# Kernel tuning notes

Hardware: AMD Instinct MI355X
Metric: run time of the kernel (lower is better)

The kernel has to match this reference:

```python
import jax, jax.numpy as jnp
import numpy as np

TEMPERATURE = 0.07
N_CLASSES = 100


def setup_inputs() -> dict:
    key = jax.random.key(0)
    k1, k2 = jax.random.split(key)
    N, D = 8192, 128
    emb = jax.random.normal(k1, (N, D), dtype=jnp.float32)
    # unit-normalize so exp(sim / temperature) stays finite in fp32
    emb = emb / jnp.linalg.norm(emb, axis=1, keepdims=True)
    labels = jax.random.randint(k2, (N,), 0, N_CLASSES, dtype=jnp.int64)
    return {"embeddings": emb, "labels": labels}


def reference(embeddings, labels):
    N = embeddings.shape[0]
    dt = embeddings.dtype
    # [N, N] similarity
    sim = jnp.matmul(embeddings, embeddings.T) / TEMPERATURE
    off_diag = 1.0 - jnp.eye(N, dtype=dt)
    pos_mask = (labels[:, None] == labels[None, :]).astype(dt) * off_diag
    exp_sim = jnp.exp(sim) * off_diag  # diagonal zeroed
    positive_sum = jnp.sum(exp_sim * pos_mask, axis=1)
    total_sum = jnp.sum(exp_sim, axis=1)
    loss = -jnp.log(positive_sum / (total_sum + 1e-8) + 1e-8)
    valid = pos_mask.sum(axis=1) > 0
    cnt = jnp.sum(valid.astype(dt))
    mean_loss = jnp.where(
        cnt > 0,
        jnp.sum(jnp.where(valid, loss, jnp.zeros_like(loss))) / jnp.maximum(cnt, 1.0),
        jnp.asarray(0.0, dtype=dt),
    )
    return mean_loss
```

## Files before the change

### kernel.cpp

```cpp
#include <hip/hip_runtime.h>

#define N 8192
#define D 128
#define SCALE_A 20.6098592f
#define NP 64
#define NBLK (NP * (NP + 1) / 2)

using short8  = __attribute__((ext_vector_type(8))) short;
using float4v = __attribute__((ext_vector_type(4))) float;

#if __has_builtin(__builtin_amdgcn_exp2f)
#define EXP2(x) __builtin_amdgcn_exp2f(x)
#else
#define EXP2(x) __expf((x) * 0.69314718f)
#endif

static __device__ inline unsigned int f2bf(float f) {
    union { float f; unsigned int u; } x;
    x.f = f;
    unsigned int u = x.u;
    return (u + 0x7FFFu + ((u >> 16) & 1u)) >> 16;
}

__global__ __launch_bounds__(256) void cl_prep(
    const float* __restrict__ emb, unsigned short* __restrict__ bfB,
    unsigned short* __restrict__ bfA, float* __restrict__ tot,
    int* __restrict__ ticket)
{
    const int t = blockIdx.x * 256 + threadIdx.x;
    const float* p = emb + (size_t)t * 16;
    uint4 ob[2], oa[2];
    #pragma unroll
    for (int h = 0; h < 2; ++h) {
        float4v f0 = *(const float4v*)(p + h * 8);
        float4v f1 = *(const float4v*)(p + h * 8 + 4);
        ob[h].x = f2bf(f0[0]) | (f2bf(f0[1]) << 16);
        ob[h].y = f2bf(f0[2]) | (f2bf(f0[3]) << 16);
        ob[h].z = f2bf(f1[0]) | (f2bf(f1[1]) << 16);
        ob[h].w = f2bf(f1[2]) | (f2bf(f1[3]) << 16);
        oa[h].x = f2bf(f0[0] * SCALE_A) | (f2bf(f0[1] * SCALE_A) << 16);
        oa[h].y = f2bf(f0[2] * SCALE_A) | (f2bf(f0[3] * SCALE_A) << 16);
        oa[h].z = f2bf(f1[0] * SCALE_A) | (f2bf(f1[1] * SCALE_A) << 16);
        oa[h].w = f2bf(f1[2] * SCALE_A) | (f2bf(f1[3] * SCALE_A) << 16);
    }
    ((uint4*)bfB)[t * 2]     = ob[0];
    ((uint4*)bfB)[t * 2 + 1] = ob[1];
    ((uint4*)bfA)[t * 2]     = oa[0];
    ((uint4*)bfA)[t * 2 + 1] = oa[1];
    if (t < 2 * N) tot[t] = 0.f;
    if (t == 0) *ticket = 0;
}

__global__ __launch_bounds__(512, 4) void cl_main(
    const unsigned short* __restrict__ bfA, const unsigned short* __restrict__ bfB,
    const int* __restrict__ labels,
    float* __restrict__ tot, float* __restrict__ pos,
    int* __restrict__ ticket, float* __restrict__ out)
{
    __shared__ uint4 ldsB[128 * 16];
    __shared__ float sred[2][8];
    __shared__ int   s_ticket;

    const int tid  = threadIdx.x;
    const int lane = tid & 63;
    const int wave = tid >> 6;
    const int q    = lane >> 4;
    const int c    = lane & 15;

    const int k = blockIdx.x;
    int bi = (int)((129.0f - sqrtf(16641.0f - 8.0f * (float)k)) * 0.5f);
    while (bi * (129 - bi) / 2 > k) --bi;
    while ((bi + 1) * (128 - bi) / 2 <= k) ++bi;
    const int bj = bi + (k - bi * (129 - bi) / 2);
    const int R0 = bi * 128, C0 = bj * 128;
    const bool diagblk = (bi == bj);

    const uint4* src = (const uint4*)bfB + (size_t)C0 * 16;
    #pragma unroll
    for (int i = 0; i < 4; ++i) {
        const int g     = tid + i * 512;
        const int row   = g >> 4;
        const int chunk = g & 15;
        __builtin_amdgcn_global_load_lds(
            (const __attribute__((address_space(1))) void*)(src + row * 16 + (chunk ^ (row & 15))),
            (__attribute__((address_space(3))) void*)(&ldsB[g]),
            16, 0, 0);
    }

    short8 afrag[4];
    int rowlab[4], collab[8];
    {
        const int arow = R0 + wave * 16 + c;
        #pragma unroll
        for (int ks = 0; ks < 4; ++ks)
            afrag[ks] = *(const short8*)(bfA + (size_t)arow * D + ks * 32 + q * 8);
        #pragma unroll
        for (int reg = 0; reg < 4; ++reg)
            rowlab[reg] = labels[R0 + wave * 16 + q * 4 + reg];
        #pragma unroll
        for (int tc = 0; tc < 8; ++tc)
            collab[tc] = labels[C0 + tc * 16 + c];
    }

    asm volatile("s_waitcnt vmcnt(0)" ::: "memory");
    __builtin_amdgcn_s_barrier();
    __builtin_amdgcn_sched_barrier(0);

    float4v acc[8];
    #pragma unroll
    for (int tc = 0; tc < 8; ++tc) {
        float4v z = {0.f, 0.f, 0.f, 0.f};
        acc[tc] = z;
    }
    const short8* ldsS = (const short8*)ldsB;
    #pragma unroll
    for (int ks = 0; ks < 4; ++ks) {
        const short8* pk = ldsS + c * 16 + ((ks * 4 + q) ^ c);
        #pragma unroll
        for (int tc = 0; tc < 8; ++tc) {
            if (diagblk && tc < wave) continue;
            short8 b = pk[tc * 256];
            acc[tc] = __builtin_amdgcn_mfma_f32_16x16x32_bf16(
                afrag[ks], b, acc[tc], 0, 0, 0);
        }
    }

    float tot_a[4] = {0.f, 0.f, 0.f, 0.f};
    float pos_a[4] = {0.f, 0.f, 0.f, 0.f};
    float ctot[8]  = {0.f, 0.f, 0.f, 0.f, 0.f, 0.f, 0.f, 0.f};
    float cpos[8]  = {0.f, 0.f, 0.f, 0.f, 0.f, 0.f, 0.f, 0.f};
    #pragma unroll
    for (int tc = 0; tc < 8; ++tc) {
        if (diagblk && tc < wave) continue;
        const int lc = collab[tc];
        if (diagblk && tc == wave) {
            #pragma unroll
            for (int reg = 0; reg < 4; ++reg) {
                float v = EXP2(acc[tc][reg]);
                if ((q * 4 + reg) >= c) v = 0.f;
                tot_a[reg] += v;  ctot[tc] += v;
                if (rowlab[reg] == lc) { pos_a[reg] += v; cpos[tc] += v; }
            }
        } else {
            #pragma unroll
            for (int reg = 0; reg < 4; ++reg) {
                float v = EXP2(acc[tc][reg]);
                tot_a[reg] += v;  ctot[tc] += v;
                if (rowlab[reg] == lc) { pos_a[reg] += v; cpos[tc] += v; }
            }
        }
    }

    #pragma unroll
    for (int reg = 0; reg < 4; ++reg) {
        float t = tot_a[reg];
        float p = pos_a[reg];
        #pragma unroll
        for (int m = 1; m < 16; m <<= 1) {
            t += __shfl_xor(t, m, 64);
            p += __shfl_xor(p, m, 64);
        }
        if (c == 0) {
            const int r = R0 + wave * 16 + q * 4 + reg;
            atomicAdd(&tot[r], t);
            atomicAdd(&pos[r], p);
        }
    }

    #pragma unroll
    for (int tc = 0; tc < 8; ++tc) {
        if (diagblk && tc < wave) continue;
        float t = ctot[tc], p = cpos[tc];
        t += __shfl_xor(t, 16, 64);  t += __shfl_xor(t, 32, 64);
        p += __shfl_xor(p, 16, 64);  p += __shfl_xor(p, 32, 64);
        if (q == 0) {
            const int cc = C0 + tc * 16 + c;
            atomicAdd(&tot[cc], t);
            atomicAdd(&pos[cc], p);
        }
    }

    asm volatile("s_waitcnt vmcnt(0)" ::: "memory");
    __syncthreads();
    if (tid == 0)
        s_ticket = __hip_atomic_fetch_add(ticket, 1, __ATOMIC_RELAXED,
                                          __HIP_MEMORY_SCOPE_AGENT);
    __syncthreads();
    if (s_ticket != NBLK - 1) return;

    float lsum = 0.f, lcnt = 0.f;
    #pragma unroll 4
    for (int i = tid; i < N; i += 512) {
        const float t = __hip_atomic_load(&tot[i], __ATOMIC_RELAXED,
                                          __HIP_MEMORY_SCOPE_AGENT);
        const float p = __hip_atomic_load(&pos[i], __ATOMIC_RELAXED,
                                          __HIP_MEMORY_SCOPE_AGENT);
        const float loss = -__logf(p / (t + 1e-8f) + 1e-8f);
        if (p > 0.f) { lsum += loss; lcnt += 1.f; }
    }
    #pragma unroll
    for (int m = 1; m < 64; m <<= 1) {
        lsum += __shfl_xor(lsum, m, 64);
        lcnt += __shfl_xor(lcnt, m, 64);
    }
    if (lane == 0) { sred[0][wave] = lsum; sred[1][wave] = lcnt; }
    __syncthreads();
    if (tid == 0) {
        float s = 0.f, n = 0.f;
        #pragma unroll
        for (int w = 0; w < 8; ++w) { s += sred[0][w]; n += sred[1][w]; }
        out[0] = (n > 0.f) ? s / fmaxf(n, 1.f) : 0.f;
    }
}

extern "C" void kernel_launch(void* const* d_in, const int* in_sizes, int n_in,
                              void* d_out, int out_size, void* d_ws, size_t ws_size,
                              hipStream_t stream) {
    const float* emb  = (const float*)d_in[0];
    const int* labels = (const int*)d_in[1];
    unsigned short* bfB = (unsigned short*)d_ws;
    unsigned short* bfA = bfB + (size_t)N * D;
    float* tot    = (float*)(bfA + (size_t)N * D);
    float* pos    = tot + N;
    int*   ticket = (int*)(pos + N);

    cl_prep<<<256, 256, 0, stream>>>(emb, bfB, bfA, tot, ticket);
    cl_main<<<NBLK, 512, 0, stream>>>(bfA, bfB, labels, tot, pos,
                                      ticket, (float*)d_out);
}
```

Measured before the change: 114.2 us.

## Make blocks persistent over row strips, reusing A fragments across column tiles

Replaces the 2080 independent upper-triangular tile blocks with 512 blocks. Each block owns one 128-row strip and walks 4–5 column tiles chosen by cyclic offset (a circulant symmetric covering), keeping the A fragments in registers and accumulating row sums across tiles. Row-sum atomics and A loads drop several-fold, and per-block launch and tile-index overhead goes away. In exchange, each block runs a serial loop where the next B tile is loaded only after the current tile is finished, with no double buffering, so load latency is exposed on every iteration. The cid==0 blocks for i<32 take one extra tile, which makes the work uneven across blocks.

```diff
diff --git a/kernel.cpp b/kernel.cpp
--- a/kernel.cpp
+++ b/kernel.cpp
@@ -4,7 +4,8 @@
 #define D 128
 #define SCALE_A 20.6098592f
 #define NP 64
-#define NBLK (NP * (NP + 1) / 2)
+#define NBLK 512
+#define NBLK_PREP 256
 
 using short8  = __attribute__((ext_vector_type(8))) short;
 using float4v = __attribute__((ext_vector_type(4))) float;
@@ -67,87 +68,138 @@
     const int q    = lane >> 4;
     const int c    = lane & 15;
 
-    const int k = blockIdx.x;
-    int bi = (int)((129.0f - sqrtf(16641.0f - 8.0f * (float)k)) * 0.5f);
-    while (bi * (129 - bi) / 2 > k) --bi;
-    while ((bi + 1) * (128 - bi) / 2 <= k) ++bi;
-    const int bj = bi + (k - bi * (129 - bi) / 2);
-    const int R0 = bi * 128, C0 = bj * 128;
-    const bool diagblk = (bi == bj);
-
-    const uint4* src = (const uint4*)bfB + (size_t)C0 * 16;
-    #pragma unroll
-    for (int i = 0; i < 4; ++i) {
-        const int g     = tid + i * 512;
-        const int row   = g >> 4;
-        const int chunk = g & 15;
-        __builtin_amdgcn_global_load_lds(
-            (const __attribute__((address_space(1))) void*)(src + row * 16 + (chunk ^ (row & 15))),
-            (__attribute__((address_space(3))) void*)(&ldsB[g]),
-            16, 0, 0);
+    const int i   = blockIdx.x >> 3;
+    const int cid = blockIdx.x & 7;
+    const int nit = (cid == 0 && i < 32) ? 5 : 4;
+    const int R0r = i * 128;
+    const uint4* bfB4 = (const uint4*)bfB;
+
+    int m0 = cid * 4;
+    {
+        const uint4* src = bfB4 + (size_t)(((i + m0) & 63) * 128) * 16;
+        #pragma unroll
+        for (int s = 0; s < 4; ++s) {
+            const int g     = tid + s * 512;
+            const int row   = g >> 4;
+            const int chunk = g & 15;
+            __builtin_amdgcn_global_load_lds(
+                (const __attribute__((address_space(1))) void*)(src + row * 16 + (chunk ^ (row & 15))),
+                (__attribute__((address_space(3))) void*)(&ldsB[g]),
+                16, 0, 0);
+        }
     }
 
     short8 afrag[4];
-    int rowlab[4], collab[8];
+    int rowlab[4];
     {
-        const int arow = R0 + wave * 16 + c;
+        const int arow = R0r + wave * 16 + c;
         #pragma unroll
         for (int ks = 0; ks < 4; ++ks)
             afrag[ks] = *(const short8*)(bfA + (size_t)arow * D + ks * 32 + q * 8);
         #pragma unroll
         for (int reg = 0; reg < 4; ++reg)
-            rowlab[reg] = labels[R0 + wave * 16 + q * 4 + reg];
-        #pragma unroll
-        for (int tc = 0; tc < 8; ++tc)
-            collab[tc] = labels[C0 + tc * 16 + c];
-    }
-
-    asm volatile("s_waitcnt vmcnt(0)" ::: "memory");
+            rowlab[reg] = labels[R0r + wave * 16 + q * 4 + reg];
+    }
+    int collab[8];
+    #pragma unroll
+    for (int tc = 0; tc < 8; ++tc)
+        collab[tc] = labels[((i + m0) & 63) * 128 + tc * 16 + c];
+
+    asm volatile("s_waitcnt vmcnt(0) lgkmcnt(0)" ::: "memory");
     __builtin_amdgcn_s_barrier();
     __builtin_amdgcn_sched_barrier(0);
 
-    float4v acc[8];
-    #pragma unroll
-    for (int tc = 0; tc < 8; ++tc) {
-        float4v z = {0.f, 0.f, 0.f, 0.f};
-        acc[tc] = z;
-    }
-    const short8* ldsS = (const short8*)ldsB;
-    #pragma unroll
-    for (int ks = 0; ks < 4; ++ks) {
-        const short8* pk = ldsS + c * 16 + ((ks * 4 + q) ^ c);
-        #pragma unroll
-        for (int tc = 0; tc < 8; ++tc) {
-            if (diagblk && tc < wave) continue;
-            short8 b = pk[tc * 256];
-            acc[tc] = __builtin_amdgcn_mfma_f32_16x16x32_bf16(
-                afrag[ks], b, acc[tc], 0, 0, 0);
-        }
-    }
-
     float tot_a[4] = {0.f, 0.f, 0.f, 0.f};
     float pos_a[4] = {0.f, 0.f, 0.f, 0.f};
-    float ctot[8]  = {0.f, 0.f, 0.f, 0.f, 0.f, 0.f, 0.f, 0.f};
-    float cpos[8]  = {0.f, 0.f, 0.f, 0.f, 0.f, 0.f, 0.f, 0.f};
-    #pragma unroll
-    for (int tc = 0; tc < 8; ++tc) {
-        if (diagblk && tc < wave) continue;
-        const int lc = collab[tc];
-        if (diagblk && tc == wave) {
+
+    #pragma unroll 1
+    for (int it = 0; it < nit; ++it) {
+        const int m    = (cid == 0) ? ((it == 4) ? 32 : it) : (cid * 4 + it);
+        const int j    = (i + m) & 63;
+        const int C0   = j * 128;
+        const bool diag = (m == 0);
+
+        float4v acc[8];
+        #pragma unroll
+        for (int tc = 0; tc < 8; ++tc) {
+            float4v z = {0.f, 0.f, 0.f, 0.f};
+            acc[tc] = z;
+        }
+        const short8* ldsS = (const short8*)ldsB;
+        #pragma unroll
+        for (int ks = 0; ks < 4; ++ks) {
+            const short8* pk = ldsS + c * 16 + ((ks * 4 + q) ^ c);
             #pragma unroll
-            for (int reg = 0; reg < 4; ++reg) {
-                float v = EXP2(acc[tc][reg]);
-                if ((q * 4 + reg) >= c) v = 0.f;
-                tot_a[reg] += v;  ctot[tc] += v;
-                if (rowlab[reg] == lc) { pos_a[reg] += v; cpos[tc] += v; }
-            }
-        } else {
+            for (int tc = 0; tc < 8; ++tc) {
+                if (diag && tc < wave) continue;
+                short8 b = pk[tc * 256];
+                acc[tc] = __builtin_amdgcn_mfma_f32_16x16x32_bf16(
+                    afrag[ks], b, acc[tc], 0, 0, 0);
+            }
+        }
+
+        float ctot[8] = {0,0,0,0,0,0,0,0};
+        float cpos[8] = {0,0,0,0,0,0,0,0};
+        #pragma unroll
+        for (int tc = 0; tc < 8; ++tc) {
+            if (diag && tc < wave) continue;
+            const int lc = collab[tc];
+            if (diag && tc == wave) {
+                #pragma unroll
+                for (int reg = 0; reg < 4; ++reg) {
+                    float v = EXP2(acc[tc][reg]);
+                    if ((q * 4 + reg) >= c) v = 0.f;
+                    tot_a[reg] += v;  ctot[tc] += v;
+                    if (rowlab[reg] == lc) { pos_a[reg] += v; cpos[tc] += v; }
+                }
+            } else {
+                #pragma unroll
+                for (int reg = 0; reg < 4; ++reg) {
+                    float v = EXP2(acc[tc][reg]);
+                    tot_a[reg] += v;  ctot[tc] += v;
+                    if (rowlab[reg] == lc) { pos_a[reg] += v; cpos[tc] += v; }
+                }
+            }
+        }
+
+        #pragma unroll
+        for (int tc = 0; tc < 8; ++tc) {
+            if (diag && tc < wave) continue;
+            float t = ctot[tc], p = cpos[tc];
+            t += __shfl_xor(t, 16, 64);  t += __shfl_xor(t, 32, 64);
+            p += __shfl_xor(p, 16, 64);  p += __shfl_xor(p, 32, 64);
+            if (q == 0) {
+                const int cc = C0 + tc * 16 + c;
+                atomicAdd(&tot[cc], t);
+                atomicAdd(&pos[cc], p);
+            }
+        }
+
+        __builtin_amdgcn_sched_barrier(0);
+        __builtin_amdgcn_s_barrier();
+        __builtin_amdgcn_sched_barrier(0);
+
+        if (it < nit - 1) {
+            const int mn = (cid == 0) ? ((it + 1 == 4) ? 32 : it + 1)
+                                      : (cid * 4 + it + 1);
+            const int jn = (i + mn) & 63;
+            const uint4* src = bfB4 + (size_t)(jn * 128) * 16;
             #pragma unroll
-            for (int reg = 0; reg < 4; ++reg) {
-                float v = EXP2(acc[tc][reg]);
-                tot_a[reg] += v;  ctot[tc] += v;
-                if (rowlab[reg] == lc) { pos_a[reg] += v; cpos[tc] += v; }
-            }
+            for (int s = 0; s < 4; ++s) {
+                const int g     = tid + s * 512;
+                const int row   = g >> 4;
+                const int chunk = g & 15;
+                __builtin_amdgcn_global_load_lds(
+                    (const __attribute__((address_space(1))) void*)(src + row * 16 + (chunk ^ (row & 15))),
+                    (__attribute__((address_space(3))) void*)(&ldsB[g]),
+                    16, 0, 0);
+            }
+            #pragma unroll
+            for (int tc = 0; tc < 8; ++tc)
+                collab[tc] = labels[jn * 128 + tc * 16 + c];
+            asm volatile("s_waitcnt vmcnt(0)" ::: "memory");
+            __builtin_amdgcn_s_barrier();
+            __builtin_amdgcn_sched_barrier(0);
         }
     }
 
@@ -161,22 +213,9 @@
             p += __shfl_xor(p, m, 64);
         }
         if (c == 0) {
-            const int r = R0 + wave * 16 + q * 4 + reg;
+            const int r = R0r + wave * 16 + q * 4 + reg;
             atomicAdd(&tot[r], t);
             atomicAdd(&pos[r], p);
-        }
-    }
-
-    #pragma unroll
-    for (int tc = 0; tc < 8; ++tc) {
-        if (diagblk && tc < wave) continue;
-        float t = ctot[tc], p = cpos[tc];
-        t += __shfl_xor(t, 16, 64);  t += __shfl_xor(t, 32, 64);
-        p += __shfl_xor(p, 16, 64);  p += __shfl_xor(p, 32, 64);
-        if (q == 0) {
-            const int cc = C0 + tc * 16 + c;
-            atomicAdd(&tot[cc], t);
-            atomicAdd(&pos[cc], p);
         }
     }
 
@@ -190,10 +229,10 @@
 
     float lsum = 0.f, lcnt = 0.f;
     #pragma unroll 4
-    for (int i = tid; i < N; i += 512) {
-        const float t = __hip_atomic_load(&tot[i], __ATOMIC_RELAXED,
+    for (int idx = tid; idx < N; idx += 512) {
+        const float t = __hip_atomic_load(&tot[idx], __ATOMIC_RELAXED,
                                           __HIP_MEMORY_SCOPE_AGENT);
-        const float p = __hip_atomic_load(&pos[i], __ATOMIC_RELAXED,
+        const float p = __hip_atomic_load(&pos[idx], __ATOMIC_RELAXED,
                                           __HIP_MEMORY_SCOPE_AGENT);
         const float loss = -__logf(p / (t + 1e-8f) + 1e-8f);
         if (p > 0.f) { lsum += loss; lcnt += 1.f; }
@@ -224,7 +263,7 @@
     float* pos    = tot + N;
     int*   ticket = (int*)(pos + N);
 
-    cl_prep<<<256, 256, 0, stream>>>(emb, bfB, bfA, tot, ticket);
+    cl_prep<<<NBLK_PREP, 256, 0, stream>>>(emb, bfB, bfA, tot, ticket);
     cl_main<<<NBLK, 512, 0, stream>>>(bfA, bfB, labels, tot, pos,
                                       ticket, (float*)d_out);
 }
```

Result: faster. 97.27 us (-14.8%).
